# Optimization experiments

Measured on AMD Instinct MI355X. Metric: run time of the kernel, lower is better.

The kernel has to match this reference:

```python
import jax, jax.numpy as jnp
import numpy as np

B, N, H, O = 262144, 64, 256, 64
MAX_ITER = 30
TOL = 1e-7
NU = 1.0


def setup_inputs() -> dict:
    key = jax.random.key(0)
    kx, kr, k1, k2, k3, k4 = jax.random.split(key, 6)
    x = jax.random.normal(kx, (B, N), dtype=jnp.float32) * 3.0
    r = jax.random.uniform(kr, (N,), dtype=jnp.float32) + 0.5  # positive rates in [0.5, 1.5)
    # MLP params (torch Linear: y = x @ W.T + b), Kaiming-ish scaling
    W1 = jax.random.normal(k1, (H, N), dtype=jnp.float32) * (1.0 / np.sqrt(N))
    b1 = jax.random.normal(k2, (H,), dtype=jnp.float32) * 0.01
    W2 = jax.random.normal(k3, (O, H), dtype=jnp.float32) * (1.0 / np.sqrt(H))
    b2 = jax.random.normal(k4, (O,), dtype=jnp.float32) * 0.01
    return {"x": x, "r": r, "W1": W1, "b1": b1, "W2": W2, "b2": b2}


def _solve_s(x, r):
    """Vectorized Newton solve of sum_i e^{-2 r_i s} x_i^2 = 1 per sample.

    Replicates solve_s_single: s starts at 0, up to MAX_ITER Newton steps,
    frozen once |F(s)| < TOL; all-zero samples return s = 0.
    """
    x2 = x * x  # [B, N]
    zero_mask = jnp.all(jnp.abs(x) <= 1e-12, axis=1)  # torch.allclose(x, 0, atol=1e-12)

    def body(_, s):
        e = jnp.exp(-2.0 * r[None, :] * s[:, None])        # [B, N]
        val = jnp.sum(e * x2, axis=1) - 1.0                # F(s)     [B]
        dval = jnp.sum(-2.0 * r[None, :] * e * x2, axis=1) # F'(s)    [B]
        safe_d = jnp.where(dval == 0.0, 1.0, dval)
        step = val / safe_d
        step = jnp.where((jnp.abs(val) < TOL) | zero_mask, 0.0, step)
        return s - step

    s0 = jnp.zeros(x.shape[0], dtype=x.dtype)
    return jax.lax.fori_loop(0, MAX_ITER, body, s0)


def reference(x, r, W1, b1, W2, b2):
    S = _solve_s(x, r)[:, None]                 # [B, 1], detached in torch (built via .item())
    S = jax.lax.stop_gradient(S)
    x_sphere = x * jnp.exp(-r[None, :] * S)     # d(-s) x
    h = jnp.maximum(x_sphere @ W1.T + b1, 0.0)  # [B, H]
    mlp_out = h @ W2.T + b2                     # [B, O]
    return mlp_out * jnp.exp(NU * S)
```

## Files before the change

### kernel.cpp

```cpp
#include <hip/hip_runtime.h>

typedef __attribute__((ext_vector_type(8))) short short8;
typedef __attribute__((ext_vector_type(4))) float floatx4;
typedef __attribute__((ext_vector_type(2))) unsigned uint2e;

static __device__ __forceinline__ unsigned short f2bf(float f) {
    unsigned u = __float_as_uint(f);
    u += 0x7FFFu + ((u >> 16) & 1u);
    return (unsigned short)(u >> 16);
}

static __device__ __forceinline__ float pl16_sum(float x) {
    unsigned u = __float_as_uint(x);
    uint2e p = __builtin_amdgcn_permlane16_swap(u, u, false, false);
    return __uint_as_float(p.x) + __uint_as_float(p.y);
}
static __device__ __forceinline__ float pl32_sum(float x) {
    unsigned u = __float_as_uint(x);
    uint2e p = __builtin_amdgcn_permlane32_swap(u, u, false, false);
    return __uint_as_float(p.x) + __uint_as_float(p.y);
}
static __device__ __forceinline__ int pl16_or(int x) {
    uint2e p = __builtin_amdgcn_permlane16_swap((unsigned)x, (unsigned)x, false, false);
    return (int)(p.x | p.y);
}
static __device__ __forceinline__ int pl32_or(int x) {
    uint2e p = __builtin_amdgcn_permlane32_swap((unsigned)x, (unsigned)x, false, false);
    return (int)(p.x | p.y);
}

__global__ __launch_bounds__(512, 2) void fused_k(const float* __restrict__ x,
                                                  const float* __restrict__ r,
                                                  const float* __restrict__ W1f,
                                                  const float* __restrict__ b1,
                                                  const float* __restrict__ W2f,
                                                  const float* __restrict__ b2,
                                                  float* __restrict__ out,
                                                  int tiles_per_block) {
    __shared__ unsigned short sW1[256 * 64];
    __shared__ unsigned short sW2[64 * 256];
    __shared__ float sB1[256];

    int tid = threadIdx.x;

    const float4* w1f4 = (const float4*)W1f;
#pragma unroll
    for (int c = 0; c < 4; ++c) {
        int g = tid + c * 512;
        int h = g >> 3, ch = g & 7;
        int prow = ((h >> 5) * 2 + ((h >> 2) & 1)) * 16 + ((h >> 3) & 3) * 4 + (h & 3);
        float4 lo = w1f4[2 * g], hi = w1f4[2 * g + 1];
        uint4 p;
        p.x = (unsigned)f2bf(lo.x) | ((unsigned)f2bf(lo.y) << 16);
        p.y = (unsigned)f2bf(lo.z) | ((unsigned)f2bf(lo.w) << 16);
        p.z = (unsigned)f2bf(hi.x) | ((unsigned)f2bf(hi.y) << 16);
        p.w = (unsigned)f2bf(hi.z) | ((unsigned)f2bf(hi.w) << 16);
        *(uint4*)&sW1[prow * 64 + (ch ^ (prow & 7)) * 8] = p;
    }
    const float4* w2f4 = (const float4*)W2f;
#pragma unroll
    for (int c = 0; c < 4; ++c) {
        int g = tid + c * 512;
        float4 lo = w2f4[2 * g], hi = w2f4[2 * g + 1];
        uint4 p;
        p.x = (unsigned)f2bf(lo.x) | ((unsigned)f2bf(lo.y) << 16);
        p.y = (unsigned)f2bf(lo.z) | ((unsigned)f2bf(lo.w) << 16);
        p.z = (unsigned)f2bf(hi.x) | ((unsigned)f2bf(hi.y) << 16);
        p.w = (unsigned)f2bf(hi.z) | ((unsigned)f2bf(hi.w) << 16);
        int row = g >> 5, ch = g & 31;
        *(uint4*)&sW2[row * 256 + (ch ^ (row & 7)) * 8] = p;
    }
    if (tid < 256) {
        int h = tid;
        int prow = ((h >> 5) * 2 + ((h >> 2) & 1)) * 16 + ((h >> 3) & 3) * 4 + (h & 3);
        sB1[prow] = b1[h];
    }
    __syncthreads();

    int wave = tid >> 6, lane = tid & 63;
    int q = lane >> 4, l16 = lane & 15;
    int sx = l16 & 7;

    float bias2[4];
#pragma unroll
    for (int n = 0; n < 4; ++n) bias2[n] = b2[n * 16 + l16];

    const float L2E2 = 2.8853900817779268f;
    float rl2[16];
    {
        const float4* r4 = (const float4*)r;
        float4 ra = r4[2 * q], rb = r4[2 * q + 1];
        float4 rc = r4[8 + 2 * q], rd = r4[8 + 2 * q + 1];
        rl2[0] = ra.x * L2E2; rl2[1] = ra.y * L2E2; rl2[2] = ra.z * L2E2; rl2[3] = ra.w * L2E2;
        rl2[4] = rb.x * L2E2; rl2[5] = rb.y * L2E2; rl2[6] = rb.z * L2E2; rl2[7] = rb.w * L2E2;
        rl2[8] = rc.x * L2E2; rl2[9] = rc.y * L2E2; rl2[10] = rc.z * L2E2; rl2[11] = rc.w * L2E2;
        rl2[12] = rd.x * L2E2; rl2[13] = rd.y * L2E2; rl2[14] = rd.z * L2E2; rl2[15] = rd.w * L2E2;
    }

    int myrow = wave * 16 + l16;
    size_t mb = (size_t)blockIdx.x * tiles_per_block * 128;
    const float4* xt = (const float4*)(x + (mb + myrow) * 64);

    float4 va = xt[2 * q], vb = xt[2 * q + 1];
    float4 vc = xt[8 + 2 * q], vd = xt[8 + 2 * q + 1];

    for (int tt = 0; tt < tiles_per_block; ++tt) {
        size_t m0 = mb + (size_t)tt * 128;

        float xv[16];
        xv[0] = va.x; xv[1] = va.y; xv[2] = va.z; xv[3] = va.w;
        xv[4] = vb.x; xv[5] = vb.y; xv[6] = vb.z; xv[7] = vb.w;
        xv[8] = vc.x; xv[9] = vc.y; xv[10] = vc.z; xv[11] = vc.w;
        xv[12] = vd.x; xv[13] = vd.y; xv[14] = vd.z; xv[15] = vd.w;

        {
            int nt = (tt + 1 < tiles_per_block) ? (tt + 1) : tt;
            const float4* xn = xt + (size_t)nt * 2048;
            va = xn[2 * q]; vb = xn[2 * q + 1];
            vc = xn[8 + 2 * q]; vd = xn[8 + 2 * q + 1];
        }

        float x2[16], rx2[16];
        float sum0 = 0.f, sumr = 0.f;
        int nz = 0;
#pragma unroll
        for (int j = 0; j < 16; ++j) {
            x2[j] = xv[j] * xv[j];
            rx2[j] = rl2[j] * x2[j];
            sum0 += x2[j];
            sumr += rx2[j];
            nz |= (fabsf(xv[j]) > 1e-12f) ? 1 : 0;
        }
        sum0 = pl32_sum(pl16_sum(sum0));
        sumr = pl32_sum(pl16_sum(sumr));
        nz = pl32_or(pl16_or(nz));

        float s = 0.f;
        if (nz) {
            s = __log2f(sum0) * sum0 * __builtin_amdgcn_rcpf(sumr);
#pragma unroll 1
            for (int it = 0; it < 10; ++it) {
                float ns = -s;
                float v = 0.f, dv = 0.f;
#pragma unroll
                for (int j = 0; j < 16; ++j) {
                    float e = __builtin_amdgcn_exp2f(ns * rl2[j]);
                    v = fmaf(e, x2[j], v);
                    dv = fmaf(e, rx2[j], dv);
                }
                v = pl32_sum(pl16_sum(v));
                dv = pl32_sum(pl16_sum(dv));
                if (__all(fabsf(v - 1.f) < 1e-5f)) break;
                s += __log2f(v) * v * __builtin_amdgcn_rcpf(dv);
            }
        }

        float hs = -0.5f * s;
        unsigned pa[8];
#pragma unroll
        for (int j = 0; j < 8; ++j) {
            float ea = xv[2 * j] * __builtin_amdgcn_exp2f(hs * rl2[2 * j]);
            float eb = xv[2 * j + 1] * __builtin_amdgcn_exp2f(hs * rl2[2 * j + 1]);
            asm("v_cvt_pk_bf16_f32 %0, %1, %2" : "=v"(pa[j]) : "v"(ea), "v"(eb));
        }
        int4 w0 = make_int4((int)pa[0], (int)pa[1], (int)pa[2], (int)pa[3]);
        int4 w1 = make_int4((int)pa[4], (int)pa[5], (int)pa[6], (int)pa[7]);
        short8 a0 = *(short8*)&w0;
        short8 a1 = *(short8*)&w1;

        float es = __builtin_amdgcn_exp2f(s * 1.4426950408889634f);
        float sc[4];
#pragma unroll
        for (int reg = 0; reg < 4; ++reg) sc[reg] = __shfl(es, q * 4 + reg);

        floatx4 oacc[4];
#pragma unroll
        for (int n = 0; n < 4; ++n)
            oacc[n] = (floatx4){bias2[n], bias2[n], bias2[n], bias2[n]};

#pragma unroll
        for (int hc = 0; hc < 8; ++hc) {
            unsigned pk0, pk1, pk2, pk3;
            {
                int t = hc * 2;
                int row = t * 16 + l16;
                short8 wb0 = *(const short8*)&sW1[row * 64 + (q ^ sx) * 8];
                short8 wb1 = *(const short8*)&sW1[row * 64 + ((q + 4) ^ sx) * 8];
                const float4 bb = *(const float4*)&sB1[t * 16 + q * 4];
                floatx4 acc = (floatx4){bb.x, bb.y, bb.z, bb.w};
                acc = __builtin_amdgcn_mfma_f32_16x16x32_bf16(wb0, a0, acc, 0, 0, 0);
                acc = __builtin_amdgcn_mfma_f32_16x16x32_bf16(wb1, a1, acc, 0, 0, 0);
                float h0 = fmaxf(acc[0], 0.f), h1 = fmaxf(acc[1], 0.f);
                float h2 = fmaxf(acc[2], 0.f), h3 = fmaxf(acc[3], 0.f);
                asm("v_cvt_pk_bf16_f32 %0, %1, %2" : "=v"(pk0) : "v"(h0), "v"(h1));
                asm("v_cvt_pk_bf16_f32 %0, %1, %2" : "=v"(pk1) : "v"(h2), "v"(h3));
            }
            {
                int t = hc * 2 + 1;
                int row = t * 16 + l16;
                short8 wb0 = *(const short8*)&sW1[row * 64 + (q ^ sx) * 8];
                short8 wb1 = *(const short8*)&sW1[row * 64 + ((q + 4) ^ sx) * 8];
                const float4 bb = *(const float4*)&sB1[t * 16 + q * 4];
                floatx4 acc = (floatx4){bb.x, bb.y, bb.z, bb.w};
                acc = __builtin_amdgcn_mfma_f32_16x16x32_bf16(wb0, a0, acc, 0, 0, 0);
                acc = __builtin_amdgcn_mfma_f32_16x16x32_bf16(wb1, a1, acc, 0, 0, 0);
                float h0 = fmaxf(acc[0], 0.f), h1 = fmaxf(acc[1], 0.f);
                float h2 = fmaxf(acc[2], 0.f), h3 = fmaxf(acc[3], 0.f);
                asm("v_cvt_pk_bf16_f32 %0, %1, %2" : "=v"(pk2) : "v"(h0), "v"(h1));
                asm("v_cvt_pk_bf16_f32 %0, %1, %2" : "=v"(pk3) : "v"(h2), "v"(h3));
            }
            int4 hw = make_int4((int)pk0, (int)pk1, (int)pk2, (int)pk3);
            short8 ha = *(short8*)&hw;
#pragma unroll
            for (int n = 0; n < 4; ++n) {
                int orow = n * 16 + l16;
                short8 wb = *(const short8*)&sW2[orow * 256 + ((hc * 4 + q) ^ sx) * 8];
                oacc[n] = __builtin_amdgcn_mfma_f32_16x16x32_bf16(ha, wb, oacc[n], 0, 0, 0);
            }
        }
#pragma unroll
        for (int n = 0; n < 4; ++n) {
#pragma unroll
            for (int reg = 0; reg < 4; ++reg) {
                out[(m0 + wave * 16 + q * 4 + reg) * 64 + n * 16 + l16] =
                    oacc[n][reg] * sc[reg];
            }
        }
    }
}

extern "C" void kernel_launch(void* const* d_in, const int* in_sizes, int n_in,
                              void* d_out, int out_size, void* d_ws, size_t ws_size,
                              hipStream_t stream) {
    const float* x  = (const float*)d_in[0];
    const float* r  = (const float*)d_in[1];
    const float* W1 = (const float*)d_in[2];
    const float* b1 = (const float*)d_in[3];
    const float* W2 = (const float*)d_in[4];
    const float* b2 = (const float*)d_in[5];
    float* out = (float*)d_out;
    int B = in_sizes[0] / 64;

    int tiles = B / 128;
    int blocks = 512;
    int tpb = tiles / blocks;

    fused_k<<<blocks, 512, 0, stream>>>(x, r, W1, b1, W2, b2, out, tpb);
}
```

Baseline: 137.3 us.

## Pre-convert weights to bf16 in a separate kernel and read W2 from global/L2

Adds a small pre-pass kernel that converts W1 and W2 to bf16 into workspace, so each block copies W1 already in bf16 instead of converting it per block. W2 is no longer staged in shared memory; the second GEMM reads its B operands straight from global memory through the cache. This halves LDS usage per block, which could raise occupancy, and cuts per-block setup work. The costs are an extra kernel launch and global/L2 load latency inside the inner MFMA loop.

```diff
diff --git a/kernel.cpp b/kernel.cpp
--- a/kernel.cpp
+++ b/kernel.cpp
@@ -29,46 +29,35 @@
     return (int)(p.x | p.y);
 }
 
+__global__ __launch_bounds__(256) void convert_w_k(const float* __restrict__ W1,
+                                                   const float* __restrict__ W2,
+                                                   unsigned short* __restrict__ w1b,
+                                                   unsigned short* __restrict__ w2b) {
+    int i = blockIdx.x * 256 + threadIdx.x;
+    w1b[i] = f2bf(W1[i]);
+    w2b[i] = f2bf(W2[i]);
+}
+
 __global__ __launch_bounds__(512, 2) void fused_k(const float* __restrict__ x,
                                                   const float* __restrict__ r,
-                                                  const float* __restrict__ W1f,
+                                                  const unsigned short* __restrict__ w1b,
                                                   const float* __restrict__ b1,
-                                                  const float* __restrict__ W2f,
+                                                  const unsigned short* __restrict__ w2b,
                                                   const float* __restrict__ b2,
                                                   float* __restrict__ out,
                                                   int tiles_per_block) {
     __shared__ unsigned short sW1[256 * 64];
-    __shared__ unsigned short sW2[64 * 256];
     __shared__ float sB1[256];
 
     int tid = threadIdx.x;
 
-    const float4* w1f4 = (const float4*)W1f;
+    const uint4* w1u = (const uint4*)w1b;
 #pragma unroll
     for (int c = 0; c < 4; ++c) {
         int g = tid + c * 512;
         int h = g >> 3, ch = g & 7;
         int prow = ((h >> 5) * 2 + ((h >> 2) & 1)) * 16 + ((h >> 3) & 3) * 4 + (h & 3);
-        float4 lo = w1f4[2 * g], hi = w1f4[2 * g + 1];
-        uint4 p;
-        p.x = (unsigned)f2bf(lo.x) | ((unsigned)f2bf(lo.y) << 16);
-        p.y = (unsigned)f2bf(lo.z) | ((unsigned)f2bf(lo.w) << 16);
-        p.z = (unsigned)f2bf(hi.x) | ((unsigned)f2bf(hi.y) << 16);
-        p.w = (unsigned)f2bf(hi.z) | ((unsigned)f2bf(hi.w) << 16);
-        *(uint4*)&sW1[prow * 64 + (ch ^ (prow & 7)) * 8] = p;
-    }
-    const float4* w2f4 = (const float4*)W2f;
-#pragma unroll
-    for (int c = 0; c < 4; ++c) {
-        int g = tid + c * 512;
-        float4 lo = w2f4[2 * g], hi = w2f4[2 * g + 1];
-        uint4 p;
-        p.x = (unsigned)f2bf(lo.x) | ((unsigned)f2bf(lo.y) << 16);
-        p.y = (unsigned)f2bf(lo.z) | ((unsigned)f2bf(lo.w) << 16);
-        p.z = (unsigned)f2bf(hi.x) | ((unsigned)f2bf(hi.y) << 16);
-        p.w = (unsigned)f2bf(hi.z) | ((unsigned)f2bf(hi.w) << 16);
-        int row = g >> 5, ch = g & 31;
-        *(uint4*)&sW2[row * 256 + (ch ^ (row & 7)) * 8] = p;
+        *(uint4*)&sW1[prow * 64 + (ch ^ (prow & 7)) * 8] = w1u[g];
     }
     if (tid < 256) {
         int h = tid;
@@ -214,7 +203,7 @@
 #pragma unroll
             for (int n = 0; n < 4; ++n) {
                 int orow = n * 16 + l16;
-                short8 wb = *(const short8*)&sW2[orow * 256 + ((hc * 4 + q) ^ sx) * 8];
+                short8 wb = *(const short8*)(w2b + orow * 256 + (hc * 4 + q) * 8);
                 oacc[n] = __builtin_amdgcn_mfma_f32_16x16x32_bf16(ha, wb, oacc[n], 0, 0, 0);
             }
         }
@@ -241,9 +230,15 @@
     float* out = (float*)d_out;
     int B = in_sizes[0] / 64;
 
+    char* ws = (char*)d_ws;
+    unsigned short* w1b = (unsigned short*)ws;
+    unsigned short* w2b = (unsigned short*)(ws + 32768);
+
+    convert_w_k<<<64, 256, 0, stream>>>(W1, W2, w1b, w2b);
+
     int tiles = B / 128;
     int blocks = 512;
     int tpb = tiles / blocks;
 
-    fused_k<<<blocks, 512, 0, stream>>>(x, r, W1, b1, W2, b2, out, tpb);
-}
+    fused_k<<<blocks, 512, 0, stream>>>(x, r, w1b, b1, w2b, b2, out, tpb);
+}
```

Result: slower. 181.3 us (+32.1%).
